# Kernel tuning notes

Hardware: AMD Instinct MI355X
Metric: run time of the kernel (lower is better)

## Reference

```python
import jax, jax.numpy as jnp
import numpy as np

N, E, B, D, L = 50000, 1600000, 128, 64, 5
BN_EPS = 1e-5

def _bn(x, g, b, m, v):
    # eval-mode BatchNorm1d with running stats
    return (x - m) * jax.lax.rsqrt(v + BN_EPS) * g + b

def setup_inputs() -> dict:
    key = jax.random.key(0)
    ks = iter(jax.random.split(key, 64))
    w = 1.0 / np.sqrt(D)
    def nrm(shape, s):
        return jax.random.normal(next(ks), shape, jnp.float32) * s
    def var(shape):
        return jax.random.uniform(next(ks), shape, jnp.float32) + 0.5
    inp = {
        "x": nrm((N, D), 1.0),
        "lin_W": nrm((D, D), w), "lin_b": nrm((D,), w),
        "eps": jnp.zeros((L,), jnp.float32),
        "gin_W1": nrm((L, D, D), w), "gin_b1": nrm((L, D), w),
        "gin_bn_g": jnp.ones((L, D), jnp.float32), "gin_bn_b": jnp.zeros((L, D), jnp.float32),
        "gin_bn_m": nrm((L, D), 0.1), "gin_bn_v": var((L, D)),
        "gin_W2": nrm((L, D, D), w), "gin_b2": nrm((L, D), w),
        "bn_g": jnp.ones((L, D), jnp.float32), "bn_b": jnp.zeros((L, D), jnp.float32),
        "bn_m": nrm((L, D), 0.1), "bn_v": var((L, D)),
        "vn_emb": jnp.zeros((D,), jnp.float32),  # init constant 0 per source
        "vn_W1": nrm((L - 1, D, D), w), "vn_b1": nrm((L - 1, D), w),
        "vn_bn1_g": jnp.ones((L - 1, D), jnp.float32), "vn_bn1_b": jnp.zeros((L - 1, D), jnp.float32),
        "vn_bn1_m": nrm((L - 1, D), 0.1), "vn_bn1_v": var((L - 1, D)),
        "vn_W2": nrm((L - 1, D, D), w), "vn_b2": nrm((L - 1, D), w),
        "vn_bn2_g": jnp.ones((L - 1, D), jnp.float32), "vn_bn2_b": jnp.zeros((L - 1, D), jnp.float32),
        "vn_bn2_m": nrm((L - 1, D), 0.1), "vn_bn2_v": var((L - 1, D)),
        "src": jax.random.randint(next(ks), (E,), 0, N, jnp.int32),
        "dst": jax.random.randint(next(ks), (E,), 0, N, jnp.int32),
        "batch_id": jnp.sort(jax.random.randint(next(ks), (N,), 0, B, jnp.int32)),
    }
    return inp

def reference(x, lin_W, lin_b, eps, gin_W1, gin_b1, gin_bn_g, gin_bn_b, gin_bn_m, gin_bn_v,
              gin_W2, gin_b2, bn_g, bn_b, bn_m, bn_v, vn_emb,
              vn_W1, vn_b1, vn_bn1_g, vn_bn1_b, vn_bn1_m, vn_bn1_v,
              vn_W2, vn_b2, vn_bn2_g, vn_bn2_b, vn_bn2_m, vn_bn2_v,
              src, dst, batch_id):
    n = x.shape[0]
    h = x @ lin_W + lin_b                       # input linear [N, D]
    h_list = [h]
    vn = jnp.broadcast_to(vn_emb, (B, D))       # per-graph virtual node [B, D]
    for l in range(L):
        h_list[l] = h_list[l] + vn[batch_id]    # virtual-node broadcast to nodes
        hl = h_list[l]
        # GINConv: sum over incoming edges of relu(src feature)
        agg = jax.ops.segment_sum(jax.nn.relu(hl[src]), dst, num_segments=n)
        z = (1.0 + eps[l]) * hl + agg
        z = z @ gin_W1[l] + gin_b1[l]
        z = jax.nn.relu(_bn(z, gin_bn_g[l], gin_bn_b[l], gin_bn_m[l], gin_bn_v[l]))
        z = z @ gin_W2[l] + gin_b2[l]
        z = _bn(z, bn_g[l], bn_b[l], bn_m[l], bn_v[l])  # outer batchnorm
        if l != L - 1:
            z = jax.nn.relu(z)                  # dropout is identity in eval mode
        h_list.append(z)
        if l < L - 1:
            # sum-pool nodes per graph, update virtual node via MLP
            vt = jax.ops.segment_sum(hl, batch_id, num_segments=B) + vn
            vt = vt @ vn_W1[l] + vn_b1[l]
            vt = jax.nn.relu(_bn(vt, vn_bn1_g[l], vn_bn1_b[l], vn_bn1_m[l], vn_bn1_v[l]))
            vt = vt @ vn_W2[l] + vn_b2[l]
            vn = jax.nn.relu(_bn(vt, vn_bn2_g[l], vn_bn2_b[l], vn_bn2_m[l], vn_bn2_v[l]))
    # JK='sum' in the source sums h_list[0..num_layers-1] (excludes final entry)
    out = h_list[0]
    for l in range(1, L):
        out = out + h_list[l]
    return out
```

## Files before the change

kernel.cpp:

```cpp
#include <hip/hip_runtime.h>

#define N_NODES 50000
#define N_EDGES 1600000
#define NB 128
#define GB 782
#define CAP 80
#define NODE_RANGE 6250
#define EDGE_BLOCKS 6250
#define INIT_BLOCKS 32

__device__ __forceinline__ unsigned short f2bf(float f) {
    unsigned u = __float_as_uint(f);
    unsigned r = (u + 0x7FFFu + ((u >> 16) & 1u)) >> 16;
    return (unsigned short)r;
}

__global__ __launch_bounds__(256) void k_build(
    const int* __restrict__ src, const int* __restrict__ dst,
    int* __restrict__ cnt, unsigned short* __restrict__ csr_src,
    const float* __restrict__ vn_emb, float* __restrict__ pooled) {
    int bid = blockIdx.x;
    if (bid >= EDGE_BLOCKS * 8) {
        int t = (bid - EDGE_BLOCKS * 8) * 256 + threadIdx.x;
        pooled[t] = vn_emb[t & 63];
        return;
    }
    int range = bid & 7;
    int e = (bid >> 3) * 256 + threadIdx.x;
    int d = dst[e];
    if (d / NODE_RANGE != range) return;
    int pos = atomicAdd(&cnt[d], 1);
    if (pos < CAP) csr_src[(size_t)d * CAP + pos] = (unsigned short)src[e];
}

__global__ __launch_bounds__(256) void k_lin_pre(
    const float* __restrict__ in, const float* __restrict__ W,
    const float* __restrict__ bias, const float* __restrict__ vn_emb,
    const int* __restrict__ batch_id,
    float* __restrict__ h, float* __restrict__ out,
    unsigned short* __restrict__ rbuf, float* __restrict__ pooled) {
    __shared__ float sW[64 * 64];
    __shared__ float sIn[64 * 68];
    int tid = threadIdx.x;
    int row0 = blockIdx.x * 64;

    const float4* W4 = (const float4*)W;
#pragma unroll
    for (int i = 0; i < 4; ++i) ((float4*)sW)[tid + 256 * i] = W4[tid + 256 * i];
    const float4* in4 = (const float4*)in;
#pragma unroll
    for (int i = 0; i < 4; ++i) {
        int idx = tid + 256 * i;
        int r = idx >> 4, j = idx & 15;
        float4 val = make_float4(0.f, 0.f, 0.f, 0.f);
        if (row0 + r < N_NODES) val = in4[(size_t)(row0 + r) * 16 + j];
        ((float4*)(sIn + r * 68))[j] = val;
    }
    __syncthreads();

    int c4 = (tid & 15) * 4;
    int rl = (tid >> 4) * 4;
    float acc[4][4] = {{0.f}};
#pragma unroll 8
    for (int k = 0; k < 64; ++k) {
        float4 wv = *(const float4*)(sW + k * 64 + c4);
        float a0 = sIn[(rl + 0) * 68 + k];
        float a1 = sIn[(rl + 1) * 68 + k];
        float a2 = sIn[(rl + 2) * 68 + k];
        float a3 = sIn[(rl + 3) * 68 + k];
        acc[0][0] += a0 * wv.x; acc[0][1] += a0 * wv.y; acc[0][2] += a0 * wv.z; acc[0][3] += a0 * wv.w;
        acc[1][0] += a1 * wv.x; acc[1][1] += a1 * wv.y; acc[1][2] += a1 * wv.z; acc[1][3] += a1 * wv.w;
        acc[2][0] += a2 * wv.x; acc[2][1] += a2 * wv.y; acc[2][2] += a2 * wv.z; acc[2][3] += a2 * wv.w;
        acc[3][0] += a3 * wv.x; acc[3][1] += a3 * wv.y; acc[3][2] += a3 * wv.z; acc[3][3] += a3 * wv.w;
    }
    float shf[4];
#pragma unroll
    for (int j = 0; j < 4; ++j) shf[j] = bias[c4 + j] + vn_emb[c4 + j];

    int lane = tid & 63;
    int wave = tid >> 6;
    int wr0 = row0 + wave * 16;
    bool full = (wr0 + 15 < N_NODES);
    bool fast = full && (batch_id[wr0] == batch_id[wr0 + 15]);
    float4 pacc = make_float4(0.f, 0.f, 0.f, 0.f);
#pragma unroll
    for (int r = 0; r < 4; ++r) {
        int row = row0 + rl + r;
        if (row >= N_NODES) continue;
        float4 v;
        v.x = acc[r][0] + shf[0];
        v.y = acc[r][1] + shf[1];
        v.z = acc[r][2] + shf[2];
        v.w = acc[r][3] + shf[3];
        *(float4*)(h + (size_t)row * 64 + c4) = v;
        *(float4*)(out + (size_t)row * 64 + c4) = v;
        ushort4 rb;
        rb.x = f2bf(fmaxf(v.x, 0.f)); rb.y = f2bf(fmaxf(v.y, 0.f));
        rb.z = f2bf(fmaxf(v.z, 0.f)); rb.w = f2bf(fmaxf(v.w, 0.f));
        *(ushort4*)(rbuf + (size_t)row * 64 + c4) = rb;
        if (fast) {
            pacc.x += v.x; pacc.y += v.y; pacc.z += v.z; pacc.w += v.w;
        } else {
            int b = batch_id[row];
            atomicAdd(&pooled[b * 64 + c4 + 0], v.x);
            atomicAdd(&pooled[b * 64 + c4 + 1], v.y);
            atomicAdd(&pooled[b * 64 + c4 + 2], v.z);
            atomicAdd(&pooled[b * 64 + c4 + 3], v.w);
        }
    }
    if (fast) {
        pacc.x += __shfl_xor(pacc.x, 16); pacc.x += __shfl_xor(pacc.x, 32);
        pacc.y += __shfl_xor(pacc.y, 16); pacc.y += __shfl_xor(pacc.y, 32);
        pacc.z += __shfl_xor(pacc.z, 16); pacc.z += __shfl_xor(pacc.z, 32);
        pacc.w += __shfl_xor(pacc.w, 16); pacc.w += __shfl_xor(pacc.w, 32);
        if ((lane >> 4) == 0) {
            int b = batch_id[wr0];
            atomicAdd(&pooled[b * 64 + c4 + 0], pacc.x);
            atomicAdd(&pooled[b * 64 + c4 + 1], pacc.y);
            atomicAdd(&pooled[b * 64 + c4 + 2], pacc.z);
            atomicAdd(&pooled[b * 64 + c4 + 3], pacc.w);
        }
    }
}

__global__ __launch_bounds__(256) void k_gin(
    const float* __restrict__ h_in, const float* __restrict__ eps, int l,
    const int* __restrict__ cnt, const unsigned short* __restrict__ csr_src,
    const unsigned short* __restrict__ rbuf_in,
    const float* __restrict__ W1, const float* __restrict__ b1,
    const float* __restrict__ g1, const float* __restrict__ be1,
    const float* __restrict__ m1, const float* __restrict__ v1,
    const float* __restrict__ W2, const float* __restrict__ b2,
    const float* __restrict__ g2, const float* __restrict__ be2,
    const float* __restrict__ m2, const float* __restrict__ v2,
    const float* __restrict__ vn, const int* __restrict__ batch_id,
    float* __restrict__ h, float* __restrict__ out,
    unsigned short* __restrict__ rbuf_out, float* __restrict__ pooled,
    int last) {
    __shared__ float sW[64 * 64];
    __shared__ float sIn[64 * 68];
    int tid = threadIdx.x;
    int row0 = blockIdx.x * 64;
    int lane = tid & 63;
    int wave = tid >> 6;

#pragma unroll
    for (int i = 0; i < 4; ++i) ((float4*)sW)[tid + 256 * i] = ((const float4*)W1)[tid + 256 * i];

    {
        int g = lane >> 3, f4 = lane & 7;
        float e1 = 1.0f + eps[l];
        const uint4* tab4 = (const uint4*)rbuf_in;
#pragma unroll 1
        for (int i = 0; i < 16; ++i) {
            int row = row0 + wave * 16 + i;
            float aL0 = 0.f, aH0 = 0.f, aL1 = 0.f, aH1 = 0.f;
            float aL2 = 0.f, aH2 = 0.f, aL3 = 0.f, aH3 = 0.f;
            if (row < N_NODES) {
                int deg = cnt[row]; if (deg > CAP) deg = CAP;
                const unsigned short* rowp = csr_src + (size_t)row * CAP;
                for (int base = 0; base < deg; base += 64) {
                    int e = base + lane;
                    int s = (e < deg) ? (int)rowp[e] : 0;
                    int c = deg - base; if (c > 64) c = 64;
                    for (int t = 0; t < c; t += 8) {
                        int idx = t + g;
                        int sj = __shfl(s, (idx < c) ? idx : t);
                        if (idx < c) {
                            uint4 u = tab4[(size_t)sj * 8 + f4];
                            aL0 += __uint_as_float(u.x << 16); aH0 += __uint_as_float(u.x & 0xFFFF0000u);
                            aL1 += __uint_as_float(u.y << 16); aH1 += __uint_as_float(u.y & 0xFFFF0000u);
                            aL2 += __uint_as_float(u.z << 16); aH2 += __uint_as_float(u.z & 0xFFFF0000u);
                            aL3 += __uint_as_float(u.w << 16); aH3 += __uint_as_float(u.w & 0xFFFF0000u);
                        }
                    }
                }
            }
#pragma unroll
            for (int off = 8; off < 64; off <<= 1) {
                aL0 += __shfl_xor(aL0, off); aH0 += __shfl_xor(aH0, off);
                aL1 += __shfl_xor(aL1, off); aH1 += __shfl_xor(aH1, off);
                aL2 += __shfl_xor(aL2, off); aH2 += __shfl_xor(aH2, off);
                aL3 += __shfl_xor(aL3, off); aH3 += __shfl_xor(aH3, off);
            }
            if (g == 0) {
                float* sp = sIn + (wave * 16 + i) * 68 + f4 * 8;
                if (row < N_NODES) {
                    const float* hp = h_in + (size_t)row * 64 + f4 * 8;
                    float4 h0 = *(const float4*)hp;
                    float4 h1 = *(const float4*)(hp + 4);
                    float4 o0, o1;
                    o0.x = e1 * h0.x + aL0; o0.y = e1 * h0.y + aH0;
                    o0.z = e1 * h0.z + aL1; o0.w = e1 * h0.w + aH1;
                    o1.x = e1 * h1.x + aL2; o1.y = e1 * h1.y + aH2;
                    o1.z = e1 * h1.z + aL3; o1.w = e1 * h1.w + aH3;
                    *(float4*)sp = o0;
                    *(float4*)(sp + 4) = o1;
                } else {
                    *(float4*)sp = make_float4(0.f, 0.f, 0.f, 0.f);
                    *(float4*)(sp + 4) = make_float4(0.f, 0.f, 0.f, 0.f);
                }
            }
        }
    }
    __syncthreads();

    int c4 = (tid & 15) * 4;
    int rl = (tid >> 4) * 4;
    float acc[4][4] = {{0.f}};
#pragma unroll 8
    for (int k = 0; k < 64; ++k) {
        float4 wv = *(const float4*)(sW + k * 64 + c4);
        float a0 = sIn[(rl + 0) * 68 + k];
        float a1 = sIn[(rl + 1) * 68 + k];
        float a2 = sIn[(rl + 2) * 68 + k];
        float a3 = sIn[(rl + 3) * 68 + k];
        acc[0][0] += a0 * wv.x; acc[0][1] += a0 * wv.y; acc[0][2] += a0 * wv.z; acc[0][3] += a0 * wv.w;
        acc[1][0] += a1 * wv.x; acc[1][1] += a1 * wv.y; acc[1][2] += a1 * wv.z; acc[1][3] += a1 * wv.w;
        acc[2][0] += a2 * wv.x; acc[2][1] += a2 * wv.y; acc[2][2] += a2 * wv.z; acc[2][3] += a2 * wv.w;
        acc[3][0] += a3 * wv.x; acc[3][1] += a3 * wv.y; acc[3][2] += a3 * wv.z; acc[3][3] += a3 * wv.w;
    }
    float scl[4], shf[4];
#pragma unroll
    for (int j = 0; j < 4; ++j) {
        int c = c4 + j;
        float sc = g1[c] * rsqrtf(v1[c] + 1e-5f);
        scl[j] = sc;
        shf[j] = be1[c] - m1[c] * sc + b1[c] * sc;
    }
    __syncthreads();
#pragma unroll
    for (int i = 0; i < 4; ++i) {
        float4 z;
        z.x = fmaxf(acc[i][0] * scl[0] + shf[0], 0.f);
        z.y = fmaxf(acc[i][1] * scl[1] + shf[1], 0.f);
        z.z = fmaxf(acc[i][2] * scl[2] + shf[2], 0.f);
        z.w = fmaxf(acc[i][3] * scl[3] + shf[3], 0.f);
        *(float4*)(sIn + (rl + i) * 68 + c4) = z;
    }
#pragma unroll
    for (int i = 0; i < 4; ++i) ((float4*)sW)[tid + 256 * i] = ((const float4*)W2)[tid + 256 * i];
    __syncthreads();

    float acc2[4][4] = {{0.f}};
#pragma unroll 8
    for (int k = 0; k < 64; ++k) {
        float4 wv = *(const float4*)(sW + k * 64 + c4);
        float a0 = sIn[(rl + 0) * 68 + k];
        float a1 = sIn[(rl + 1) * 68 + k];
        float a2 = sIn[(rl + 2) * 68 + k];
        float a3 = sIn[(rl + 3) * 68 + k];
        acc2[0][0] += a0 * wv.x; acc2[0][1] += a0 * wv.y; acc2[0][2] += a0 * wv.z; acc2[0][3] += a0 * wv.w;
        acc2[1][0] += a1 * wv.x; acc2[1][1] += a1 * wv.y; acc2[1][2] += a1 * wv.z; acc2[1][3] += a1 * wv.w;
        acc2[2][0] += a2 * wv.x; acc2[2][1] += a2 * wv.y; acc2[2][2] += a2 * wv.z; acc2[2][3] += a2 * wv.w;
        acc2[3][0] += a3 * wv.x; acc2[3][1] += a3 * wv.y; acc2[3][2] += a3 * wv.z; acc2[3][3] += a3 * wv.w;
    }
#pragma unroll
    for (int j = 0; j < 4; ++j) {
        int c = c4 + j;
        float sc = g2[c] * rsqrtf(v2[c] + 1e-5f);
        scl[j] = sc;
        shf[j] = be2[c] - m2[c] * sc + b2[c] * sc;
    }

    int wr0 = row0 + wave * 16;
    bool full = (wr0 + 15 < N_NODES);
    bool fast = (!last) && full && (batch_id[wr0] == batch_id[wr0 + 15]);
    float4 pacc = make_float4(0.f, 0.f, 0.f, 0.f);
#pragma unroll
    for (int r = 0; r < 4; ++r) {
        int row = row0 + rl + r;
        if (row >= N_NODES) continue;
        int b = batch_id[row];
        float4 vv = *(const float4*)(vn + b * 64 + c4);
        float4 v;
        v.x = fmaxf(acc2[r][0] * scl[0] + shf[0], 0.f) + vv.x;
        v.y = fmaxf(acc2[r][1] * scl[1] + shf[1], 0.f) + vv.y;
        v.z = fmaxf(acc2[r][2] * scl[2] + shf[2], 0.f) + vv.z;
        v.w = fmaxf(acc2[r][3] * scl[3] + shf[3], 0.f) + vv.w;
        float4 o = *(const float4*)(out + (size_t)row * 64 + c4);
        o.x += v.x; o.y += v.y; o.z += v.z; o.w += v.w;
        *(float4*)(out + (size_t)row * 64 + c4) = o;
        if (!last) {
            *(float4*)(h + (size_t)row * 64 + c4) = v;
            ushort4 rb;
            rb.x = f2bf(fmaxf(v.x, 0.f)); rb.y = f2bf(fmaxf(v.y, 0.f));
            rb.z = f2bf(fmaxf(v.z, 0.f)); rb.w = f2bf(fmaxf(v.w, 0.f));
            *(ushort4*)(rbuf_out + (size_t)row * 64 + c4) = rb;
            if (fast) {
                pacc.x += v.x; pacc.y += v.y; pacc.z += v.z; pacc.w += v.w;
            } else {
                atomicAdd(&pooled[b * 64 + c4 + 0], v.x);
                atomicAdd(&pooled[b * 64 + c4 + 1], v.y);
                atomicAdd(&pooled[b * 64 + c4 + 2], v.z);
                atomicAdd(&pooled[b * 64 + c4 + 3], v.w);
            }
        }
    }
    if (fast) {
        pacc.x += __shfl_xor(pacc.x, 16); pacc.x += __shfl_xor(pacc.x, 32);
        pacc.y += __shfl_xor(pacc.y, 16); pacc.y += __shfl_xor(pacc.y, 32);
        pacc.z += __shfl_xor(pacc.z, 16); pacc.z += __shfl_xor(pacc.z, 32);
        pacc.w += __shfl_xor(pacc.w, 16); pacc.w += __shfl_xor(pacc.w, 32);
        if ((lane >> 4) == 0) {
            int b = batch_id[wr0];
            atomicAdd(&pooled[b * 64 + c4 + 0], pacc.x);
            atomicAdd(&pooled[b * 64 + c4 + 1], pacc.y);
            atomicAdd(&pooled[b * 64 + c4 + 2], pacc.z);
            atomicAdd(&pooled[b * 64 + c4 + 3], pacc.w);
        }
    }
}

__global__ __launch_bounds__(1024) void k_vnmlp(
    const float* __restrict__ pooled_in,
    const float* __restrict__ W1, const float* __restrict__ b1,
    const float* __restrict__ g1, const float* __restrict__ be1,
    const float* __restrict__ m1, const float* __restrict__ v1,
    const float* __restrict__ W2, const float* __restrict__ b2,
    const float* __restrict__ g2, const float* __restrict__ be2,
    const float* __restrict__ m2, const float* __restrict__ v2,
    float* __restrict__ vn_out, float* __restrict__ pooled_out) {
    __shared__ float sP[128 * 68];
    __shared__ float sW[64 * 64];
    int tid = threadIdx.x;

    ((float4*)sW)[tid] = ((const float4*)W1)[tid];
#pragma unroll
    for (int i = 0; i < 2; ++i) {
        int idx = tid + 1024 * i;
        int r = idx >> 4, j = idx & 15;
        ((float4*)(sP + r * 68))[j] = ((const float4*)pooled_in)[idx];
    }
    __syncthreads();

    int c4 = (tid & 15) * 4, rg = tid >> 4;
    float acc[2][4] = {{0.f}};
#pragma unroll 8
    for (int k = 0; k < 64; ++k) {
        float4 w = *(const float4*)(sW + k * 64 + c4);
#pragma unroll
        for (int i = 0; i < 2; ++i) {
            float a = sP[(rg * 2 + i) * 68 + k];
            acc[i][0] += a * w.x; acc[i][1] += a * w.y;
            acc[i][2] += a * w.z; acc[i][3] += a * w.w;
        }
    }
    float scl[4], shf[4];
#pragma unroll
    for (int j = 0; j < 4; ++j) {
        int c = c4 + j;
        float sc = g1[c] * rsqrtf(v1[c] + 1e-5f);
        scl[j] = sc;
        shf[j] = be1[c] - m1[c] * sc + b1[c] * sc;
    }
    __syncthreads();
#pragma unroll
    for (int i = 0; i < 2; ++i) {
        float4 z;
        z.x = fmaxf(acc[i][0] * scl[0] + shf[0], 0.f);
        z.y = fmaxf(acc[i][1] * scl[1] + shf[1], 0.f);
        z.z = fmaxf(acc[i][2] * scl[2] + shf[2], 0.f);
        z.w = fmaxf(acc[i][3] * scl[3] + shf[3], 0.f);
        *(float4*)(sP + (rg * 2 + i) * 68 + c4) = z;
    }
    ((float4*)sW)[tid] = ((const float4*)W2)[tid];
    __syncthreads();

    float acc2[2][4] = {{0.f}};
#pragma unroll 8
    for (int k = 0; k < 64; ++k) {
        float4 w = *(const float4*)(sW + k * 64 + c4);
#pragma unroll
        for (int i = 0; i < 2; ++i) {
            float a = sP[(rg * 2 + i) * 68 + k];
            acc2[i][0] += a * w.x; acc2[i][1] += a * w.y;
            acc2[i][2] += a * w.z; acc2[i][3] += a * w.w;
        }
    }
#pragma unroll
    for (int j = 0; j < 4; ++j) {
        int c = c4 + j;
        float sc = g2[c] * rsqrtf(v2[c] + 1e-5f);
        scl[j] = sc;
        shf[j] = be2[c] - m2[c] * sc + b2[c] * sc;
    }
#pragma unroll
    for (int i = 0; i < 2; ++i) {
        int row = rg * 2 + i;
        float4 o;
        o.x = fmaxf(acc2[i][0] * scl[0] + shf[0], 0.f);
        o.y = fmaxf(acc2[i][1] * scl[1] + shf[1], 0.f);
        o.z = fmaxf(acc2[i][2] * scl[2] + shf[2], 0.f);
        o.w = fmaxf(acc2[i][3] * scl[3] + shf[3], 0.f);
        *(float4*)(vn_out + row * 64 + c4) = o;
        *(float4*)(pooled_out + row * 64 + c4) = o;
    }
}

extern "C" void kernel_launch(void* const* d_in, const int* in_sizes, int n_in,
                              void* d_out, int out_size, void* d_ws, size_t ws_size,
                              hipStream_t stream) {
    const float* x      = (const float*)d_in[0];
    const float* lin_W  = (const float*)d_in[1];
    const float* lin_b  = (const float*)d_in[2];
    const float* eps    = (const float*)d_in[3];
    const float* gin_W1 = (const float*)d_in[4];
    const float* gin_b1 = (const float*)d_in[5];
    const float* gbn_g  = (const float*)d_in[6];
    const float* gbn_b  = (const float*)d_in[7];
    const float* gbn_m  = (const float*)d_in[8];
    const float* gbn_v  = (const float*)d_in[9];
    const float* gin_W2 = (const float*)d_in[10];
    const float* gin_b2 = (const float*)d_in[11];
    const float* bn_g   = (const float*)d_in[12];
    const float* bn_b   = (const float*)d_in[13];
    const float* bn_m   = (const float*)d_in[14];
    const float* bn_v   = (const float*)d_in[15];
    const float* vn_emb = (const float*)d_in[16];
    const float* vn_W1  = (const float*)d_in[17];
    const float* vn_b1  = (const float*)d_in[18];
    const float* v1g    = (const float*)d_in[19];
    const float* v1b    = (const float*)d_in[20];
    const float* v1m    = (const float*)d_in[21];
    const float* v1v    = (const float*)d_in[22];
    const float* vn_W2  = (const float*)d_in[23];
    const float* vn_b2  = (const float*)d_in[24];
    const float* v2g    = (const float*)d_in[25];
    const float* v2b    = (const float*)d_in[26];
    const float* v2m    = (const float*)d_in[27];
    const float* v2v    = (const float*)d_in[28];
    const int* src      = (const int*)d_in[29];
    const int* dst      = (const int*)d_in[30];
    const int* batch_id = (const int*)d_in[31];
    float* out = (float*)d_out;

    float* h      = (float*)d_ws;
    unsigned short* rbufA = (unsigned short*)(h + (size_t)N_NODES * 64);
    unsigned short* rbufB = rbufA + (size_t)N_NODES * 64;
    float* vn     = (float*)(rbufB + (size_t)N_NODES * 64);
    float* pooled = vn  + (size_t)NB * 64;
    int*   cnt    = (int*)(pooled + (size_t)NB * 64);
    unsigned short* csr_src = (unsigned short*)(cnt + N_NODES);

    hipMemsetAsync(cnt, 0, N_NODES * sizeof(int), stream);
    k_build<<<EDGE_BLOCKS * 8 + INIT_BLOCKS, 256, 0, stream>>>(src, dst, cnt, csr_src,
                                                               vn_emb, pooled);

    k_lin_pre<<<GB, 256, 0, stream>>>(x, lin_W, lin_b, vn_emb, batch_id,
                                      h, out, rbufA, pooled);

    for (int l = 0; l < 4; ++l) {
        unsigned short* rin  = (l & 1) ? rbufB : rbufA;
        unsigned short* rout = (l & 1) ? rbufA : rbufB;
        k_vnmlp<<<1, 1024, 0, stream>>>(pooled,
                                        vn_W1 + l * 4096, vn_b1 + l * 64,
                                        v1g + l * 64, v1b + l * 64, v1m + l * 64, v1v + l * 64,
                                        vn_W2 + l * 4096, vn_b2 + l * 64,
                                        v2g + l * 64, v2b + l * 64, v2m + l * 64, v2v + l * 64,
                                        vn, pooled);
        k_gin<<<GB, 256, 0, stream>>>(h, eps, l, cnt, csr_src, rin,
                                      gin_W1 + l * 4096, gin_b1 + l * 64,
                                      gbn_g + l * 64, gbn_b + l * 64,
                                      gbn_m + l * 64, gbn_v + l * 64,
                                      gin_W2 + l * 4096, gin_b2 + l * 64,
                                      bn_g + l * 64, bn_b + l * 64,
                                      bn_m + l * 64, bn_v + l * 64,
                                      vn, batch_id, h, out, rout, pooled,
                                      l == 3);
    }
}
```

Measured before the change: 545.3 us.

## Assign one node per 8-lane group in GIN gather with 512-thread blocks

The GIN kernel moves to 512 threads per block. Each 8-lane group of a wave now owns a whole destination row, so a wave processes eight rows in parallel. Previously a wave walked its 16 rows one at a time and reduced partial sums with cross-lane shuffles. Each group now loops serially over its row's edges, reading four neighbour indices at once with a vector load and unrolling the gathers, which removes the shuffle broadcast and reduction. The matmul stage is re-tiled to two rows per thread to match. The trade-offs are load imbalance between groups with different degrees and higher register pressure under the larger block size.

```diff
diff --git a/kernel.cpp b/kernel.cpp
--- a/kernel.cpp
+++ b/kernel.cpp
@@ -123,7 +123,7 @@
     }
 }
 
-__global__ __launch_bounds__(256) void k_gin(
+__global__ __launch_bounds__(512) void k_gin(
     const float* __restrict__ h_in, const float* __restrict__ eps, int l,
     const int* __restrict__ cnt, const unsigned short* __restrict__ csr_src,
     const unsigned short* __restrict__ rbuf_in,
@@ -145,80 +145,80 @@
     int wave = tid >> 6;
 
 #pragma unroll
-    for (int i = 0; i < 4; ++i) ((float4*)sW)[tid + 256 * i] = ((const float4*)W1)[tid + 256 * i];
+    for (int i = 0; i < 2; ++i)
+        ((float4*)sW)[tid + 512 * i] = ((const float4*)W1)[tid + 512 * i];
 
     {
         int g = lane >> 3, f4 = lane & 7;
+        int row = row0 + wave * 8 + g;
         float e1 = 1.0f + eps[l];
         const uint4* tab4 = (const uint4*)rbuf_in;
-#pragma unroll 1
-        for (int i = 0; i < 16; ++i) {
-            int row = row0 + wave * 16 + i;
-            float aL0 = 0.f, aH0 = 0.f, aL1 = 0.f, aH1 = 0.f;
-            float aL2 = 0.f, aH2 = 0.f, aL3 = 0.f, aH3 = 0.f;
-            if (row < N_NODES) {
-                int deg = cnt[row]; if (deg > CAP) deg = CAP;
-                const unsigned short* rowp = csr_src + (size_t)row * CAP;
-                for (int base = 0; base < deg; base += 64) {
-                    int e = base + lane;
-                    int s = (e < deg) ? (int)rowp[e] : 0;
-                    int c = deg - base; if (c > 64) c = 64;
-                    for (int t = 0; t < c; t += 8) {
-                        int idx = t + g;
-                        int sj = __shfl(s, (idx < c) ? idx : t);
-                        if (idx < c) {
-                            uint4 u = tab4[(size_t)sj * 8 + f4];
-                            aL0 += __uint_as_float(u.x << 16); aH0 += __uint_as_float(u.x & 0xFFFF0000u);
-                            aL1 += __uint_as_float(u.y << 16); aH1 += __uint_as_float(u.y & 0xFFFF0000u);
-                            aL2 += __uint_as_float(u.z << 16); aH2 += __uint_as_float(u.z & 0xFFFF0000u);
-                            aL3 += __uint_as_float(u.w << 16); aH3 += __uint_as_float(u.w & 0xFFFF0000u);
-                        }
-                    }
-                }
+        float aL0 = 0.f, aH0 = 0.f, aL1 = 0.f, aH1 = 0.f;
+        float aL2 = 0.f, aH2 = 0.f, aL3 = 0.f, aH3 = 0.f;
+        if (row < N_NODES) {
+            int deg = cnt[row]; if (deg > CAP) deg = CAP;
+            const unsigned short* rowp = csr_src + (size_t)row * CAP;
+            int e = 0;
+            for (; e + 3 < deg; e += 4) {
+                ushort4 s4 = *(const ushort4*)(rowp + e);
+                uint4 u0 = tab4[(size_t)s4.x * 8 + f4];
+                uint4 u1 = tab4[(size_t)s4.y * 8 + f4];
+                uint4 u2 = tab4[(size_t)s4.z * 8 + f4];
+                uint4 u3 = tab4[(size_t)s4.w * 8 + f4];
+                aL0 += __uint_as_float(u0.x << 16); aH0 += __uint_as_float(u0.x & 0xFFFF0000u);
+                aL1 += __uint_as_float(u0.y << 16); aH1 += __uint_as_float(u0.y & 0xFFFF0000u);
+                aL2 += __uint_as_float(u0.z << 16); aH2 += __uint_as_float(u0.z & 0xFFFF0000u);
+                aL3 += __uint_as_float(u0.w << 16); aH3 += __uint_as_float(u0.w & 0xFFFF0000u);
+                aL0 += __uint_as_float(u1.x << 16); aH0 += __uint_as_float(u1.x & 0xFFFF0000u);
+                aL1 += __uint_as_float(u1.y << 16); aH1 += __uint_as_float(u1.y & 0xFFFF0000u);
+                aL2 += __uint_as_float(u1.z << 16); aH2 += __uint_as_float(u1.z & 0xFFFF0000u);
+                aL3 += __uint_as_float(u1.w << 16); aH3 += __uint_as_float(u1.w & 0xFFFF0000u);
+                aL0 += __uint_as_float(u2.x << 16); aH0 += __uint_as_float(u2.x & 0xFFFF0000u);
+                aL1 += __uint_as_float(u2.y << 16); aH1 += __uint_as_float(u2.y & 0xFFFF0000u);
+                aL2 += __uint_as_float(u2.z << 16); aH2 += __uint_as_float(u2.z & 0xFFFF0000u);
+                aL3 += __uint_as_float(u2.w << 16); aH3 += __uint_as_float(u2.w & 0xFFFF0000u);
+                aL0 += __uint_as_float(u3.x << 16); aH0 += __uint_as_float(u3.x & 0xFFFF0000u);
+                aL1 += __uint_as_float(u3.y << 16); aH1 += __uint_as_float(u3.y & 0xFFFF0000u);
+                aL2 += __uint_as_float(u3.z << 16); aH2 += __uint_as_float(u3.z & 0xFFFF0000u);
+                aL3 += __uint_as_float(u3.w << 16); aH3 += __uint_as_float(u3.w & 0xFFFF0000u);
             }
-#pragma unroll
-            for (int off = 8; off < 64; off <<= 1) {
-                aL0 += __shfl_xor(aL0, off); aH0 += __shfl_xor(aH0, off);
-                aL1 += __shfl_xor(aL1, off); aH1 += __shfl_xor(aH1, off);
-                aL2 += __shfl_xor(aL2, off); aH2 += __shfl_xor(aH2, off);
-                aL3 += __shfl_xor(aL3, off); aH3 += __shfl_xor(aH3, off);
+            for (; e < deg; ++e) {
+                uint4 u = tab4[(size_t)rowp[e] * 8 + f4];
+                aL0 += __uint_as_float(u.x << 16); aH0 += __uint_as_float(u.x & 0xFFFF0000u);
+                aL1 += __uint_as_float(u.y << 16); aH1 += __uint_as_float(u.y & 0xFFFF0000u);
+                aL2 += __uint_as_float(u.z << 16); aH2 += __uint_as_float(u.z & 0xFFFF0000u);
+                aL3 += __uint_as_float(u.w << 16); aH3 += __uint_as_float(u.w & 0xFFFF0000u);
             }
-            if (g == 0) {
-                float* sp = sIn + (wave * 16 + i) * 68 + f4 * 8;
-                if (row < N_NODES) {
-                    const float* hp = h_in + (size_t)row * 64 + f4 * 8;
-                    float4 h0 = *(const float4*)hp;
-                    float4 h1 = *(const float4*)(hp + 4);
-                    float4 o0, o1;
-                    o0.x = e1 * h0.x + aL0; o0.y = e1 * h0.y + aH0;
-                    o0.z = e1 * h0.z + aL1; o0.w = e1 * h0.w + aH1;
-                    o1.x = e1 * h1.x + aL2; o1.y = e1 * h1.y + aH2;
-                    o1.z = e1 * h1.z + aL3; o1.w = e1 * h1.w + aH3;
-                    *(float4*)sp = o0;
-                    *(float4*)(sp + 4) = o1;
-                } else {
-                    *(float4*)sp = make_float4(0.f, 0.f, 0.f, 0.f);
-                    *(float4*)(sp + 4) = make_float4(0.f, 0.f, 0.f, 0.f);
-                }
-            }
+        }
+        float* sp = sIn + (wave * 8 + g) * 68 + f4 * 8;
+        if (row < N_NODES) {
+            const float* hp = h_in + (size_t)row * 64 + f4 * 8;
+            float4 h0 = *(const float4*)hp;
+            float4 h1 = *(const float4*)(hp + 4);
+            float4 o0, o1;
+            o0.x = e1 * h0.x + aL0; o0.y = e1 * h0.y + aH0;
+            o0.z = e1 * h0.z + aL1; o0.w = e1 * h0.w + aH1;
+            o1.x = e1 * h1.x + aL2; o1.y = e1 * h1.y + aH2;
+            o1.z = e1 * h1.z + aL3; o1.w = e1 * h1.w + aH3;
+            *(float4*)sp = o0;
+            *(float4*)(sp + 4) = o1;
+        } else {
+            *(float4*)sp = make_float4(0.f, 0.f, 0.f, 0.f);
+            *(float4*)(sp + 4) = make_float4(0.f, 0.f, 0.f, 0.f);
         }
     }
     __syncthreads();
 
     int c4 = (tid & 15) * 4;
-    int rl = (tid >> 4) * 4;
-    float acc[4][4] = {{0.f}};
+    int rg = tid >> 4;
+    float acc[2][4] = {{0.f}};
 #pragma unroll 8
     for (int k = 0; k < 64; ++k) {
         float4 wv = *(const float4*)(sW + k * 64 + c4);
-        float a0 = sIn[(rl + 0) * 68 + k];
-        float a1 = sIn[(rl + 1) * 68 + k];
-        float a2 = sIn[(rl + 2) * 68 + k];
-        float a3 = sIn[(rl + 3) * 68 + k];
+        float a0 = sIn[(2 * rg + 0) * 68 + k];
+        float a1 = sIn[(2 * rg + 1) * 68 + k];
         acc[0][0] += a0 * wv.x; acc[0][1] += a0 * wv.y; acc[0][2] += a0 * wv.z; acc[0][3] += a0 * wv.w;
         acc[1][0] += a1 * wv.x; acc[1][1] += a1 * wv.y; acc[1][2] += a1 * wv.z; acc[1][3] += a1 * wv.w;
-        acc[2][0] += a2 * wv.x; acc[2][1] += a2 * wv.y; acc[2][2] += a2 * wv.z; acc[2][3] += a2 * wv.w;
-        acc[3][0] += a3 * wv.x; acc[3][1] += a3 * wv.y; acc[3][2] += a3 * wv.z; acc[3][3] += a3 * wv.w;
     }
     float scl[4], shf[4];
 #pragma unroll
@@ -230,30 +230,27 @@
     }
     __syncthreads();
 #pragma unroll
-    for (int i = 0; i < 4; ++i) {
+    for (int i = 0; i < 2; ++i) {
         float4 z;
         z.x = fmaxf(acc[i][0] * scl[0] + shf[0], 0.f);
         z.y = fmaxf(acc[i][1] * scl[1] + shf[1], 0.f);
         z.z = fmaxf(acc[i][2] * scl[2] + shf[2], 0.f);
         z.w = fmaxf(acc[i][3] * scl[3] + shf[3], 0.f);
-        *(float4*)(sIn + (rl + i) * 68 + c4) = z;
-    }
-#pragma unroll
-    for (int i = 0; i < 4; ++i) ((float4*)sW)[tid + 256 * i] = ((const float4*)W2)[tid + 256 * i];
-    __syncthreads();
-
-    float acc2[4][4] = {{0.f}};
+        *(float4*)(sIn + (2 * rg + i) * 68 + c4) = z;
+    }
+#pragma unroll
+    for (int i = 0; i < 2; ++i)
+        ((float4*)sW)[tid + 512 * i] = ((const float4*)W2)[tid + 512 * i];
+    __syncthreads();
+
+    float acc2[2][4] = {{0.f}};
 #pragma unroll 8
     for (int k = 0; k < 64; ++k) {
         float4 wv = *(const float4*)(sW + k * 64 + c4);
-        float a0 = sIn[(rl + 0) * 68 + k];
-        float a1 = sIn[(rl + 1) * 68 + k];
-        float a2 = sIn[(rl + 2) * 68 + k];
-        float a3 = sIn[(rl + 3) * 68 + k];
+        float a0 = sIn[(2 * rg + 0) * 68 + k];
+        float a1 = sIn[(2 * rg + 1) * 68 + k];
         acc2[0][0] += a0 * wv.x; acc2[0][1] += a0 * wv.y; acc2[0][2] += a0 * wv.z; acc2[0][3] += a0 * wv.w;
         acc2[1][0] += a1 * wv.x; acc2[1][1] += a1 * wv.y; acc2[1][2] += a1 * wv.z; acc2[1][3] += a1 * wv.w;
-        acc2[2][0] += a2 * wv.x; acc2[2][1] += a2 * wv.y; acc2[2][2] += a2 * wv.z; acc2[2][3] += a2 * wv.w;
-        acc2[3][0] += a3 * wv.x; acc2[3][1] += a3 * wv.y; acc2[3][2] += a3 * wv.z; acc2[3][3] += a3 * wv.w;
     }
 #pragma unroll
     for (int j = 0; j < 4; ++j) {
@@ -263,13 +260,13 @@
         shf[j] = be2[c] - m2[c] * sc + b2[c] * sc;
     }
 
-    int wr0 = row0 + wave * 16;
-    bool full = (wr0 + 15 < N_NODES);
-    bool fast = (!last) && full && (batch_id[wr0] == batch_id[wr0 + 15]);
+    int wr0 = row0 + wave * 8;
+    bool full = (wr0 + 7 < N_NODES);
+    bool fast = (!last) && full && (batch_id[wr0] == batch_id[wr0 + 7]);
     float4 pacc = make_float4(0.f, 0.f, 0.f, 0.f);
 #pragma unroll
-    for (int r = 0; r < 4; ++r) {
-        int row = row0 + rl + r;
+    for (int r = 0; r < 2; ++r) {
+        int row = row0 + rg * 2 + r;
         if (row >= N_NODES) continue;
         int b = batch_id[row];
         float4 vv = *(const float4*)(vn + b * 64 + c4);
@@ -459,7 +456,7 @@
                                         vn_W2 + l * 4096, vn_b2 + l * 64,
                                         v2g + l * 64, v2b + l * 64, v2m + l * 64, v2v + l * 64,
                                         vn, pooled);
-        k_gin<<<GB, 256, 0, stream>>>(h, eps, l, cnt, csr_src, rin,
+        k_gin<<<GB, 512, 0, stream>>>(h, eps, l, cnt, csr_src, rin,
                                       gin_W1 + l * 4096, gin_b1 + l * 64,
                                       gbn_g + l * 64, gbn_b + l * 64,
                                       gbn_m + l * 64, gbn_v + l * 64,
```

New measurement: 485.1 us. -11.0%, faster.
